# Optimization experiments

Measured on AMD Instinct MI355X. Metric: run time of the kernel, lower is better.

## Reference

```python
import jax, jax.numpy as jnp
import numpy as np

B, S, D, H = 2, 2048, 1024, 16
DK = D // H
ALPHA = 0.5


def setup_inputs() -> dict:
    key = jax.random.key(0)
    ks = jax.random.split(key, 16)
    scale = 0.02
    return {
        "q": jax.random.normal(ks[0], (B, S, D), dtype=jnp.float32),
        "k": jax.random.normal(ks[1], (B, S, D), dtype=jnp.float32),
        "v": jax.random.normal(ks[2], (B, S, D), dtype=jnp.float32),
        "attn_mask": jax.random.randint(ks[3], (S, S), 0, 2, dtype=jnp.int32),
        "causal_mask": jax.random.uniform(ks[4], (S, S), dtype=jnp.float32),
        "Wq": jax.random.normal(ks[5], (D, D), dtype=jnp.float32) * scale,
        "bq": jnp.zeros((D,), dtype=jnp.float32),
        "Wk": jax.random.normal(ks[6], (D, D), dtype=jnp.float32) * scale,
        "bk": jnp.zeros((D,), dtype=jnp.float32),
        "Wv": jax.random.normal(ks[7], (D, D), dtype=jnp.float32) * scale,
        "bv": jnp.zeros((D,), dtype=jnp.float32),
        "Wo": jax.random.normal(ks[8], (D, D), dtype=jnp.float32) * scale,
        "bo": jnp.zeros((D,), dtype=jnp.float32),
    }


def _split_heads(x):
    # [B, S, D] -> [B, H, S, DK]
    return x.reshape(B, S, H, DK).transpose(0, 2, 1, 3)


def reference(q, k, v, attn_mask, causal_mask, Wq, bq, Wk, bk, Wv, bv, Wo, bo):
    qh = _split_heads(q @ Wq.T + bq)
    kh = _split_heads(k @ Wk.T + bk)
    vh = _split_heads(v @ Wv.T + bv)
    scores = jnp.einsum("bhqd,bhkd->bhqk", qh, kh) / jnp.sqrt(jnp.float32(DK))
    # additive mask: positions where attn_mask == 1 get -1e9 (broadcast [S,S] -> [B,H,S,S])
    scores = jnp.where(attn_mask[None, None] == 1, jnp.float32(-1e9), scores)
    # multiplicative causal scaling (applied AFTER the fill, as in the original)
    scores = scores * (1.0 + ALPHA * causal_mask[None, None])
    probs = jax.nn.softmax(scores, axis=-1)  # dropout is identity in eval / p=0
    attn = jnp.einsum("bhqk,bhkd->bhqd", probs, vh)  # [B, H, S, DK]
    concat = attn.transpose(0, 2, 1, 3).reshape(B, S, D)
    out = concat @ Wo.T + bo
    return (out, attn)
```

## Files before the change

kernel.cpp:

```cpp
#include <hip/hip_runtime.h>
#include <hip/hip_bf16.h>

#define NB 2
#define NS 2048
#define ND 1024
#define NH 16
#define NDK 64
#define GK 1024

using bf16_t = __hip_bfloat16;
typedef __attribute__((ext_vector_type(8))) short bf16x8;
typedef __attribute__((ext_vector_type(4))) float f32x4;
typedef unsigned short u16;
typedef unsigned int u32;

#define SC_LOG2E 0.1803368801f

static __device__ __forceinline__ u16 f2bf(float f) {
    __hip_bfloat16 h = __float2bfloat16(f);
    return *reinterpret_cast<u16*>(&h);
}

static __device__ __forceinline__ u32 cvtpk2(float a, float b) {
    u32 r;
    asm("v_cvt_pk_bf16_f32 %0, %1, %2" : "=v"(r) : "v"(a), "v"(b));
    return r;
}

#define GLDS16(gp, lp)                                                                    \
    __builtin_amdgcn_global_load_lds((const __attribute__((address_space(1))) void*)(gp), \
                                     (__attribute__((address_space(3))) void*)(lp), 16, 0, 0)

struct PrepArgs {
    const float* qkv_s[3];
    u16* qkv_d[3];
    const float* w_s[4];
    u16* w_d[4];
    const int* am;
    const float* cm;
    float* comb;
};

__global__ __launch_bounds__(256) void prep_kernel(PrepArgs a) {
    const int x = blockIdx.x, y = blockIdx.y, tid = threadIdx.x;
    if (y < 3) {
        int i = x * 256 + tid;
        float4 v = reinterpret_cast<const float4*>(a.qkv_s[y])[i];
        ushort4 o;
        o.x = f2bf(v.x); o.y = f2bf(v.y); o.z = f2bf(v.z); o.w = f2bf(v.w);
        reinterpret_cast<ushort4*>(a.qkv_d[y])[i] = o;
    } else if (y == 3) {
        int w = x >> 10;
        int i = (x & 1023) * 256 + tid;
        float4 v = reinterpret_cast<const float4*>(a.w_s[w])[i];
        ushort4 o;
        o.x = f2bf(v.x); o.y = f2bf(v.y); o.z = f2bf(v.z); o.w = f2bf(v.w);
        reinterpret_cast<ushort4*>(a.w_d[w])[i] = o;
    } else {
        int i = (x * 256 + tid) * 4;
        int4 m = *reinterpret_cast<const int4*>(a.am + i);
        float4 c = *reinterpret_cast<const float4*>(a.cm + i);
        float4 r;
        r.x = (m.x == 1) ? -1.0f : fmaf(0.5f * SC_LOG2E, c.x, SC_LOG2E);
        r.y = (m.y == 1) ? -1.0f : fmaf(0.5f * SC_LOG2E, c.y, SC_LOG2E);
        r.z = (m.z == 1) ? -1.0f : fmaf(0.5f * SC_LOG2E, c.z, SC_LOG2E);
        r.w = (m.w == 1) ? -1.0f : fmaf(0.5f * SC_LOG2E, c.w, SC_LOG2E);
        *reinterpret_cast<float4*>(a.comb + i) = r;
    }
}

struct MMArgs {
    const u16* A;
    const u16* W;
    const float* bias;
    void* out;
    int mode;
};

template <int BN>
__global__ __launch_bounds__(256) void mm_glds(MMArgs g0, MMArgs g1, MMArgs g2) {
    const MMArgs ga = (blockIdx.z == 0) ? g0 : (blockIdx.z == 1) ? g1 : g2;
    constexpr int BM = 128, BK = 32;
    constexpr int JN = BN / 32;
    __shared__ __align__(16) u16 As[2][BM * BK];
    __shared__ __align__(16) u16 Bs[2][BN * BK];

    const int tid = threadIdx.x;
    const int lane = tid & 63;
    const int w = tid >> 6;
    const int wm = w >> 1, wn = w & 1;
    const int fr = lane & 15, fg = lane >> 4;

    const int nxy = gridDim.x * gridDim.y;
    const int flat0 = blockIdx.y * gridDim.x + blockIdx.x;
    const int chunk = nxy >> 3;
    const int flat = (flat0 & 7) * chunk + (flat0 >> 3);
    const int bxi = flat % gridDim.x, byi = flat / gridDim.x;
    const int bm0 = byi * BM, bn0 = bxi * BN;

    const u16* agp = ga.A + (size_t)(bm0 + w * 32 + (lane >> 2)) * GK + (lane & 3) * 8;
    const u16* bgp = ga.W +
                     (size_t)(bn0 + w * (BN == 128 ? 32 : 16) + (lane >> 2)) * GK +
                     (lane & 3) * 8;

    f32x4 acc[4][JN];
    const f32x4 z4 = {0.f, 0.f, 0.f, 0.f};
#pragma unroll
    for (int i = 0; i < 4; ++i)
#pragma unroll
        for (int j = 0; j < JN; ++j) acc[i][j] = z4;

    {
        u16* la = &As[0][w * 1024];
        u16* lb = &Bs[0][w * (BN == 128 ? 1024 : 512)];
        GLDS16(agp, la);
        GLDS16(agp + 16 * GK, la + 512);
        if (BN == 128) {
            GLDS16(bgp, lb);
            GLDS16(bgp + 16 * GK, lb + 512);
        } else {
            GLDS16(bgp, lb);
        }
    }
    __syncthreads();

    int cur = 0;
    for (int kt = 0; kt < GK / BK; ++kt) {
        if (kt + 1 < GK / BK) {
            const int ko = (kt + 1) * BK;
            u16* la = &As[cur ^ 1][w * 1024];
            u16* lb = &Bs[cur ^ 1][w * (BN == 128 ? 1024 : 512)];
            GLDS16(agp + ko, la);
            GLDS16(agp + ko + 16 * GK, la + 512);
            if (BN == 128) {
                GLDS16(bgp + ko, lb);
                GLDS16(bgp + ko + 16 * GK, lb + 512);
            } else {
                GLDS16(bgp + ko, lb);
            }
        }
        bf16x8 af[4], bfr[JN];
#pragma unroll
        for (int i = 0; i < 4; ++i)
            af[i] = *(const bf16x8*)&As[cur][(wm * 64 + i * 16 + fr) * BK + fg * 8];
#pragma unroll
        for (int j = 0; j < JN; ++j)
            bfr[j] = *(const bf16x8*)&Bs[cur][(wn * (BN / 2) + j * 16 + fr) * BK + fg * 8];
#pragma unroll
        for (int i = 0; i < 4; ++i)
#pragma unroll
            for (int j = 0; j < JN; ++j)
                acc[i][j] = __builtin_amdgcn_mfma_f32_16x16x32_bf16(af[i], bfr[j], acc[i][j],
                                                                    0, 0, 0);
        __syncthreads();
        cur ^= 1;
    }

#pragma unroll
    for (int j = 0; j < JN; ++j) {
        const int col = bn0 + wn * (BN / 2) + j * 16 + fr;
        const float bv_ = ga.bias[col];
        if (ga.mode == 2) {
            const int h_ = col >> 6, dk = col & (NDK - 1);
#pragma unroll
            for (int i = 0; i < 4; ++i) {
                const int row0 = bm0 + wm * 64 + i * 16 + fg * 4;
                const int b_ = row0 >> 11, s_ = row0 & (NS - 1);
                uint2 pw;
                pw.x = cvtpk2(acc[i][j][0] + bv_, acc[i][j][1] + bv_);
                pw.y = cvtpk2(acc[i][j][2] + bv_, acc[i][j][3] + bv_);
                *(uint2*)((u16*)ga.out +
                          (((size_t)(b_ * NH + h_)) * NDK + dk) * NS + s_) = pw;
            }
        } else {
#pragma unroll
            for (int i = 0; i < 4; ++i) {
#pragma unroll
                for (int r = 0; r < 4; ++r) {
                    const int row = bm0 + wm * 64 + i * 16 + fg * 4 + r;
                    const float val = acc[i][j][r] + bv_;
                    if (ga.mode == 1) {
                        const int b_ = row >> 11, s_ = row & (NS - 1);
                        const int h_ = col >> 6, dk = col & (NDK - 1);
                        ((bf16_t*)ga.out)[(((size_t)(b_ * NH + h_)) * NS + s_) * NDK + dk] =
                            __float2bfloat16(val);
                    } else {
                        ((float*)ga.out)[(size_t)row * ND + col] = val;
                    }
                }
            }
        }
    }
}

__global__ __launch_bounds__(256) void flash_mfma(const u16* __restrict__ Qh,
                                                  const u16* __restrict__ Kh,
                                                  const u16* __restrict__ VhT,
                                                  const float* __restrict__ comb,
                                                  float* __restrict__ attnOut,
                                                  u16* __restrict__ concatOut) {
    __shared__ __align__(16) char smem[40960];

    const int tid = threadIdx.x;
    const int w = tid >> 6;
    const int lane = tid & 63;
    const int qc = lane & 15;
    const int g = lane >> 4;
    const int bh = blockIdx.y;
    const int b_ = bh >> 4, h_ = bh & 15;
    const int qw = blockIdx.x * 64 + w * 16;

    const size_t bhoff = (size_t)bh * NS * NDK;

    const u32 kxl = qc & 3;
    const u32 kx2 = (qc >> 2) & 1;

    const int srow = lane >> 3;
    const int sblk = (lane & 7) ^ srow;
    const u16* kgp = Kh + bhoff + (size_t)(w * 16 + srow) * NDK + sblk * 8;
    const u16* vgp = VhT + bhoff + (size_t)(w * 16 + srow) * NS + sblk * 8;
    char* kdst = smem + w * 2048;
    char* vdst = smem + 16384 + w * 2048;

    bf16x8 qf0, qf1;
    {
        const u16* qp = Qh + bhoff + (size_t)(qw + qc) * NDK + g * 8;
        qf0 = *(const bf16x8*)(qp);
        qf1 = *(const bf16x8*)(qp + 32);
    }

    bf16x8 vones;
#pragma unroll
    for (int j = 0; j < 8; ++j) vones[j] = (short)0x3F80;

    const f32x4 z4 = {0.f, 0.f, 0.f, 0.f};
    f32x4 o[4];
    o[0] = o[1] = o[2] = o[3] = z4;
    f32x4 o_l = z4;

    const u32 cA = kx2 << 6;
    const u32 cB = cA ^ 64;
    const u32 laneRC = (u32)qc * 128 + ((g ^ kxl) << 4);
    const char* kb0 = smem + laneRC + cA;
    const char* kb1 = smem + laneRC + cB;
    const char* vb0 = smem + 16384 + laneRC + cA;
    const char* vb1 = smem + 16384 + laneRC + cB;
    char* ptrow = smem + 32768 + w * 2048 + qc * 128;
    const char* prd0 = ptrow + ((g ^ kxl) << 4) + cA;
    const char* prd1 = ptrow + ((g ^ kxl) << 4) + cB;
    char* pwb = ptrow + (u32)((g * 8) ^ ((qc & 1) << 4));
    const u32 sxb = (u32)((qc >> 1) & 3) << 5;

    const float* cbp = comb + (size_t)(qw + qc) * NS + g * 4;

    GLDS16(kgp, kdst);
    GLDS16(kgp + 8 * NDK, kdst + 1024);
    GLDS16(vgp, vdst);
    GLDS16(vgp + 8 * NS, vdst + 1024);
    const u16* kgn = kgp + 64 * NDK;
    const u16* vgn = vgp + 64;
    __syncthreads();

    u32 koff = 0;
    for (int kt = 0; kt < NS; kt += 64) {
        if (kt + 64 < NS) {
            char* kd = kdst + (koff ^ 8192);
            char* vd = vdst + (koff ^ 8192);
            GLDS16(kgn, kd);
            GLDS16(kgn + 8 * NDK, kd + 1024);
            GLDS16(vgn, vd);
            GLDS16(vgn + 8 * NS, vd + 1024);
            kgn += 64 * NDK;
            vgn += 64;
        }

        f32x4 s[4];
        s[0] = s[1] = s[2] = s[3] = z4;
#pragma unroll
        for (int ks = 0; ks < 4; ++ks) {
            bf16x8 kf0 = *(const bf16x8*)(kb0 + koff + ks * 2048);
            bf16x8 kf1 = *(const bf16x8*)(kb1 + koff + ks * 2048);
            s[ks] = __builtin_amdgcn_mfma_f32_16x16x32_bf16(kf0, qf0, s[ks], 0, 0, 0);
            s[ks] = __builtin_amdgcn_mfma_f32_16x16x32_bf16(kf1, qf1, s[ks], 0, 0, 0);
        }

#pragma unroll
        for (int ks = 0; ks < 4; ++ks) {
            float4 c4 = *(const float4*)(cbp + ks * 16);
            const float* cc = (const float*)&c4;
            float p0 = __builtin_amdgcn_exp2f(s[ks][0] * cc[0]);
            float p1 = __builtin_amdgcn_exp2f(s[ks][1] * cc[1]);
            float p2 = __builtin_amdgcn_exp2f(s[ks][2] * cc[2]);
            float p3 = __builtin_amdgcn_exp2f(s[ks][3] * cc[3]);
            p0 = (cc[0] < 0.f) ? 0.f : p0;
            p1 = (cc[1] < 0.f) ? 0.f : p1;
            p2 = (cc[2] < 0.f) ? 0.f : p2;
            p3 = (cc[3] < 0.f) ? 0.f : p3;
            uint2 pw;
            pw.x = cvtpk2(p0, p1);
            pw.y = cvtpk2(p2, p3);
            *(uint2*)(pwb + (((u32)(ks * 32)) ^ sxb)) = pw;
        }
        cbp += 64;

        asm volatile("s_waitcnt lgkmcnt(0)" ::: "memory");
        __builtin_amdgcn_sched_barrier(0);

        bf16x8 pf0 = *(const bf16x8*)(prd0);
        bf16x8 pf1 = *(const bf16x8*)(prd1);
        o_l = __builtin_amdgcn_mfma_f32_16x16x32_bf16(pf0, vones, o_l, 0, 0, 0);
        o_l = __builtin_amdgcn_mfma_f32_16x16x32_bf16(pf1, vones, o_l, 0, 0, 0);
#pragma unroll
        for (int dsub = 0; dsub < 4; ++dsub) {
            bf16x8 vf0 = *(const bf16x8*)(vb0 + koff + dsub * 2048);
            bf16x8 vf1 = *(const bf16x8*)(vb1 + koff + dsub * 2048);
            o[dsub] = __builtin_amdgcn_mfma_f32_16x16x32_bf16(pf0, vf0, o[dsub], 0, 0, 0);
            o[dsub] = __builtin_amdgcn_mfma_f32_16x16x32_bf16(pf1, vf1, o[dsub], 0, 0, 0);
        }
        __syncthreads();
        koff ^= 8192;
    }

    float inv[4];
#pragma unroll
    for (int r = 0; r < 4; ++r) inv[r] = 1.0f / o_l[r];

#pragma unroll
    for (int dsub = 0; dsub < 4; ++dsub) {
#pragma unroll
        for (int r = 0; r < 4; ++r) {
            const float val = o[dsub][r] * inv[r];
            const int qg = qw + g * 4 + r;
            const int d = dsub * 16 + qc;
            attnOut[bhoff + (size_t)qg * NDK + d] = val;
            concatOut[((size_t)b_ * NS + qg) * ND + h_ * NDK + d] = f2bf(val);
        }
    }
}

extern "C" void kernel_launch(void* const* d_in, const int* in_sizes, int n_in,
                              void* d_out, int out_size, void* d_ws, size_t ws_size,
                              hipStream_t stream) {
    const float* q = (const float*)d_in[0];
    const float* k = (const float*)d_in[1];
    const float* v = (const float*)d_in[2];
    const int* am = (const int*)d_in[3];
    const float* cm = (const float*)d_in[4];
    const float* Wq = (const float*)d_in[5];
    const float* bq = (const float*)d_in[6];
    const float* Wk = (const float*)d_in[7];
    const float* bk = (const float*)d_in[8];
    const float* Wv = (const float*)d_in[9];
    const float* bv = (const float*)d_in[10];
    const float* Wo = (const float*)d_in[11];
    const float* bo = (const float*)d_in[12];

    float* out = (float*)d_out;
    float* attn_out = out + (size_t)NB * NS * ND;

    char* p = (char*)d_ws;
    float* CB = (float*)p;  p += (size_t)NS * NS * 4;
    u16* qb = (u16*)p;      p += (size_t)NB * NS * ND * 2;
    u16* kb_ = (u16*)p;     p += (size_t)NB * NS * ND * 2;
    u16* vb_ = (u16*)p;     p += (size_t)NB * NS * ND * 2;
    u16* Wqb = (u16*)p;     p += (size_t)ND * ND * 2;
    u16* Wkb = (u16*)p;     p += (size_t)ND * ND * 2;
    u16* Wvb = (u16*)p;     p += (size_t)ND * ND * 2;
    u16* Wob = (u16*)p;     p += (size_t)ND * ND * 2;
    u16* Qh = (u16*)p;      p += (size_t)NB * NS * ND * 2;
    u16* Kh = (u16*)p;      p += (size_t)NB * NS * ND * 2;
    u16* VhT = (u16*)p;     p += (size_t)NB * NS * ND * 2;
    u16* CCb = (u16*)p;     p += (size_t)NB * NS * ND * 2;

    PrepArgs pa;
    pa.qkv_s[0] = q;  pa.qkv_d[0] = qb;
    pa.qkv_s[1] = k;  pa.qkv_d[1] = kb_;
    pa.qkv_s[2] = v;  pa.qkv_d[2] = vb_;
    pa.w_s[0] = Wq;   pa.w_d[0] = Wqb;
    pa.w_s[1] = Wk;   pa.w_d[1] = Wkb;
    pa.w_s[2] = Wv;   pa.w_d[2] = Wvb;
    pa.w_s[3] = Wo;   pa.w_d[3] = Wob;
    pa.am = am;
    pa.cm = cm;
    pa.comb = CB;
    hipLaunchKernelGGL(prep_kernel, dim3(4096, 5), dim3(256), 0, stream, pa);

    MMArgs mq = {qb, Wqb, bq, (void*)Qh, 1};
    MMArgs mk = {kb_, Wkb, bk, (void*)Kh, 1};
    MMArgs mv = {vb_, Wvb, bv, (void*)VhT, 2};
    hipLaunchKernelGGL((mm_glds<128>), dim3(ND / 128, 4096 / 128, 3), dim3(256), 0, stream,
                       mq, mk, mv);

    hipLaunchKernelGGL(flash_mfma, dim3(NS / 64, NB * NH), dim3(256), 0, stream, Qh, Kh, VhT,
                       CB, attn_out, CCb);

    MMArgs mo = {CCb, Wob, bo, (void*)out, 0};
    hipLaunchKernelGGL((mm_glds<64>), dim3(ND / 64, 4096 / 128, 1), dim3(256), 0, stream,
                       mo, mo, mo);
}
```

Measured before the change: 165.6 us.

## Restructure flash loop into 32-key phases with four-stage K/V ring buffer

```diff
diff --git a/kernel.cpp b/kernel.cpp
--- a/kernel.cpp
+++ b/kernel.cpp
@@ -199,7 +199,7 @@
                                                   const float* __restrict__ comb,
                                                   float* __restrict__ attnOut,
                                                   u16* __restrict__ concatOut) {
-    __shared__ __align__(16) char smem[40960];
+    __shared__ __align__(16) char smem[36864];
 
     const int tid = threadIdx.x;
     const int w = tid >> 6;
@@ -214,13 +214,16 @@
 
     const u32 kxl = qc & 3;
     const u32 kx2 = (qc >> 2) & 1;
-
-    const int srow = lane >> 3;
-    const int sblk = (lane & 7) ^ srow;
-    const u16* kgp = Kh + bhoff + (size_t)(w * 16 + srow) * NDK + sblk * 8;
-    const u16* vgp = VhT + bhoff + (size_t)(w * 16 + srow) * NS + sblk * 8;
-    char* kdst = smem + w * 2048;
-    char* vdst = smem + 16384 + w * 2048;
+    const u32 px = (qc >> 1) & 3;
+
+    const int ksr = lane >> 3;
+    const int ksb = (lane & 7) ^ ksr;
+    const u16* kgn = Kh + bhoff + (size_t)(w * 8 + ksr) * NDK + ksb * 8;
+    const int vsr = lane >> 2;
+    const int vsb = (lane & 3) ^ (vsr & 3);
+    const u16* vgn = VhT + bhoff + (size_t)(w * 16 + vsr) * NS + vsb * 8;
+    char* ksm = smem + w * 1024;
+    char* vsm = smem + 16384 + w * 1024;
 
     bf16x8 qf0, qf1;
     {
@@ -238,88 +241,106 @@
     o[0] = o[1] = o[2] = o[3] = z4;
     f32x4 o_l = z4;
 
-    const u32 cA = kx2 << 6;
-    const u32 cB = cA ^ 64;
-    const u32 laneRC = (u32)qc * 128 + ((g ^ kxl) << 4);
-    const char* kb0 = smem + laneRC + cA;
-    const char* kb1 = smem + laneRC + cB;
-    const char* vb0 = smem + 16384 + laneRC + cA;
-    const char* vb1 = smem + 16384 + laneRC + cB;
-    char* ptrow = smem + 32768 + w * 2048 + qc * 128;
-    const char* prd0 = ptrow + ((g ^ kxl) << 4) + cA;
-    const char* prd1 = ptrow + ((g ^ kxl) << 4) + cB;
-    char* pwb = ptrow + (u32)((g * 8) ^ ((qc & 1) << 4));
-    const u32 sxb = (u32)((qc >> 1) & 3) << 5;
+    const char* kb0 = smem + qc * 128 + ((g ^ kxl) << 4) + (kx2 << 6);
+    const char* kb1 = smem + qc * 128 + ((g ^ kxl) << 4) + ((kx2 ^ 1) << 6);
+    const char* vb = smem + 16384 + qc * 64 + ((g ^ kxl) << 4);
+    char* ptrow = smem + 32768 + w * 1024 + qc * 64;
+    char* pwb0 = ptrow + ((((g >> 1) ^ px) & 3) << 4) + ((g & 1) << 3);
+    char* pwb1 = ptrow + (((((g >> 1) | 2) ^ px) & 3) << 4) + ((g & 1) << 3);
+    const char* prd = ptrow + (((g ^ px) & 3) << 4);
 
     const float* cbp = comb + (size_t)(qw + qc) * NS + g * 4;
 
-    GLDS16(kgp, kdst);
-    GLDS16(kgp + 8 * NDK, kdst + 1024);
-    GLDS16(vgp, vdst);
-    GLDS16(vgp + 8 * NS, vdst + 1024);
-    const u16* kgn = kgp + 64 * NDK;
-    const u16* vgn = vgp + 64;
-    __syncthreads();
-
-    u32 koff = 0;
-    for (int kt = 0; kt < NS; kt += 64) {
-        if (kt + 64 < NS) {
-            char* kd = kdst + (koff ^ 8192);
-            char* vd = vdst + (koff ^ 8192);
-            GLDS16(kgn, kd);
-            GLDS16(kgn + 8 * NDK, kd + 1024);
-            GLDS16(vgn, vd);
-            GLDS16(vgn + 8 * NS, vd + 1024);
-            kgn += 64 * NDK;
-            vgn += 64;
-        }
-
-        f32x4 s[4];
-        s[0] = s[1] = s[2] = s[3] = z4;
-#pragma unroll
-        for (int ks = 0; ks < 4; ++ks) {
-            bf16x8 kf0 = *(const bf16x8*)(kb0 + koff + ks * 2048);
-            bf16x8 kf1 = *(const bf16x8*)(kb1 + koff + ks * 2048);
-            s[ks] = __builtin_amdgcn_mfma_f32_16x16x32_bf16(kf0, qf0, s[ks], 0, 0, 0);
-            s[ks] = __builtin_amdgcn_mfma_f32_16x16x32_bf16(kf1, qf1, s[ks], 0, 0, 0);
-        }
-
-#pragma unroll
-        for (int ks = 0; ks < 4; ++ks) {
-            float4 c4 = *(const float4*)(cbp + ks * 16);
-            const float* cc = (const float*)&c4;
-            float p0 = __builtin_amdgcn_exp2f(s[ks][0] * cc[0]);
-            float p1 = __builtin_amdgcn_exp2f(s[ks][1] * cc[1]);
-            float p2 = __builtin_amdgcn_exp2f(s[ks][2] * cc[2]);
-            float p3 = __builtin_amdgcn_exp2f(s[ks][3] * cc[3]);
-            p0 = (cc[0] < 0.f) ? 0.f : p0;
-            p1 = (cc[1] < 0.f) ? 0.f : p1;
-            p2 = (cc[2] < 0.f) ? 0.f : p2;
-            p3 = (cc[3] < 0.f) ? 0.f : p3;
-            uint2 pw;
-            pw.x = cvtpk2(p0, p1);
-            pw.y = cvtpk2(p2, p3);
-            *(uint2*)(pwb + (((u32)(ks * 32)) ^ sxb)) = pw;
-        }
-        cbp += 64;
-
-        asm volatile("s_waitcnt lgkmcnt(0)" ::: "memory");
-        __builtin_amdgcn_sched_barrier(0);
-
-        bf16x8 pf0 = *(const bf16x8*)(prd0);
-        bf16x8 pf1 = *(const bf16x8*)(prd1);
-        o_l = __builtin_amdgcn_mfma_f32_16x16x32_bf16(pf0, vones, o_l, 0, 0, 0);
-        o_l = __builtin_amdgcn_mfma_f32_16x16x32_bf16(pf1, vones, o_l, 0, 0, 0);
-#pragma unroll
-        for (int dsub = 0; dsub < 4; ++dsub) {
-            bf16x8 vf0 = *(const bf16x8*)(vb0 + koff + dsub * 2048);
-            bf16x8 vf1 = *(const bf16x8*)(vb1 + koff + dsub * 2048);
-            o[dsub] = __builtin_amdgcn_mfma_f32_16x16x32_bf16(pf0, vf0, o[dsub], 0, 0, 0);
-            o[dsub] = __builtin_amdgcn_mfma_f32_16x16x32_bf16(pf1, vf1, o[dsub], 0, 0, 0);
-        }
-        __syncthreads();
-        koff ^= 8192;
-    }
+    float4 cX0, cX1, cY0, cY1;
+
+    cX0 = *(const float4*)(cbp);
+    cX1 = *(const float4*)(cbp + 16);
+    cbp += 32;
+    GLDS16(kgn, ksm);
+    GLDS16(vgn, vsm);
+    kgn += 32 * NDK; vgn += 32;
+    GLDS16(kgn, ksm + 4096);
+    GLDS16(vgn, vsm + 4096);
+    kgn += 32 * NDK; vgn += 32;
+    GLDS16(kgn, ksm + 8192);
+    GLDS16(vgn, vsm + 8192);
+    kgn += 32 * NDK; vgn += 32;
+    asm volatile("s_waitcnt vmcnt(4)" ::: "memory");
+    __builtin_amdgcn_s_barrier();
+    asm volatile("" ::: "memory");
+
+#define FL_PHASE(KOFF, KOFFW, CC0, CC1, CN0, CN1)                                          \
+    {                                                                                      \
+        CN0 = *(const float4*)(cbp);                                                       \
+        CN1 = *(const float4*)(cbp + 16);                                                  \
+        cbp += 32;                                                                         \
+        GLDS16(kgn, ksm + (KOFFW));                                                        \
+        GLDS16(vgn, vsm + (KOFFW));                                                        \
+        kgn += 32 * NDK;                                                                   \
+        vgn += 32;                                                                         \
+        f32x4 s0 = z4, s1 = z4;                                                            \
+        {                                                                                  \
+            bf16x8 a0 = *(const bf16x8*)(kb0 + (KOFF));                                    \
+            bf16x8 a1 = *(const bf16x8*)(kb1 + (KOFF));                                    \
+            s0 = __builtin_amdgcn_mfma_f32_16x16x32_bf16(a0, qf0, s0, 0, 0, 0);            \
+            s0 = __builtin_amdgcn_mfma_f32_16x16x32_bf16(a1, qf1, s0, 0, 0, 0);            \
+            bf16x8 b0 = *(const bf16x8*)(kb0 + (KOFF) + 2048);                             \
+            bf16x8 b1 = *(const bf16x8*)(kb1 + (KOFF) + 2048);                             \
+            s1 = __builtin_amdgcn_mfma_f32_16x16x32_bf16(b0, qf0, s1, 0, 0, 0);            \
+            s1 = __builtin_amdgcn_mfma_f32_16x16x32_bf16(b1, qf1, s1, 0, 0, 0);            \
+        }                                                                                  \
+        {                                                                                  \
+            float p0 = __builtin_amdgcn_exp2f(s0[0] * (CC0).x);                            \
+            float p1 = __builtin_amdgcn_exp2f(s0[1] * (CC0).y);                            \
+            float p2 = __builtin_amdgcn_exp2f(s0[2] * (CC0).z);                            \
+            float p3 = __builtin_amdgcn_exp2f(s0[3] * (CC0).w);                            \
+            p0 = ((CC0).x < 0.f) ? 0.f : p0;                                               \
+            p1 = ((CC0).y < 0.f) ? 0.f : p1;                                               \
+            p2 = ((CC0).z < 0.f) ? 0.f : p2;                                               \
+            p3 = ((CC0).w < 0.f) ? 0.f : p3;                                               \
+            uint2 pwa;                                                                     \
+            pwa.x = cvtpk2(p0, p1);                                                        \
+            pwa.y = cvtpk2(p2, p3);                                                        \
+            *(uint2*)(pwb0) = pwa;                                                         \
+            float q0 = __builtin_amdgcn_exp2f(s1[0] * (CC1).x);                            \
+            float q1 = __builtin_amdgcn_exp2f(s1[1] * (CC1).y);                            \
+            float q2 = __builtin_amdgcn_exp2f(s1[2] * (CC1).z);                            \
+            float q3 = __builtin_amdgcn_exp2f(s1[3] * (CC1).w);                            \
+            q0 = ((CC1).x < 0.f) ? 0.f : q0;                                               \
+            q1 = ((CC1).y < 0.f) ? 0.f : q1;                                               \
+            q2 = ((CC1).z < 0.f) ? 0.f : q2;                                               \
+            q3 = ((CC1).w < 0.f) ? 0.f : q3;                                               \
+            uint2 pwbv;                                                                    \
+            pwbv.x = cvtpk2(q0, q1);                                                       \
+            pwbv.y = cvtpk2(q2, q3);                                                       \
+            *(uint2*)(pwb1) = pwbv;                                                        \
+        }                                                                                  \
+        asm volatile("s_waitcnt lgkmcnt(0)" ::: "memory");                                 \
+        __builtin_amdgcn_sched_barrier(0);                                                 \
+        {                                                                                  \
+            bf16x8 pf = *(const bf16x8*)(prd);                                             \
+            o_l = __builtin_amdgcn_mfma_f32_16x16x32_bf16(pf, vones, o_l, 0, 0, 0);        \
+            bf16x8 v0 = *(const bf16x8*)(vb + (KOFF));                                     \
+            o[0] = __builtin_amdgcn_mfma_f32_16x16x32_bf16(pf, v0, o[0], 0, 0, 0);         \
+            bf16x8 v1 = *(const bf16x8*)(vb + (KOFF) + 1024);                              \
+            o[1] = __builtin_amdgcn_mfma_f32_16x16x32_bf16(pf, v1, o[1], 0, 0, 0);         \
+            bf16x8 v2 = *(const bf16x8*)(vb + (KOFF) + 2048);                              \
+            o[2] = __builtin_amdgcn_mfma_f32_16x16x32_bf16(pf, v2, o[2], 0, 0, 0);         \
+            bf16x8 v3 = *(const bf16x8*)(vb + (KOFF) + 3072);                              \
+            o[3] = __builtin_amdgcn_mfma_f32_16x16x32_bf16(pf, v3, o[3], 0, 0, 0);         \
+        }                                                                                  \
+        asm volatile("s_waitcnt vmcnt(6)" ::: "memory");                                   \
+        __builtin_amdgcn_s_barrier();                                                      \
+        asm volatile("" ::: "memory");                                                     \
+    }
+
+    for (int it = 0; it < 16; ++it) {
+        FL_PHASE(0, 12288, cX0, cX1, cY0, cY1)
+        FL_PHASE(4096, 0, cY0, cY1, cX0, cX1)
+        FL_PHASE(8192, 4096, cX0, cX1, cY0, cY1)
+        FL_PHASE(12288, 8192, cY0, cY1, cX0, cX1)
+    }
+#undef FL_PHASE
 
     float inv[4];
 #pragma unroll
```

After: 169.0 us. 1.02x slower.
